# Performance work log

Measured on AMD Instinct MI355X. Metric: run time of the kernel, lower is better.

## Reference

```python
import jax, jax.numpy as jnp
import numpy as np

B, L, D, H = 1, 2048, 1024, 16
d = D // H  # head dim = 64


def setup_inputs() -> dict:
    key = jax.random.key(0)
    ks = jax.random.split(key, 8)
    s = 1.0 / np.sqrt(D)
    return {
        "x": jax.random.normal(ks[0], (B, L, D), jnp.float32),
        "Wqkv_w": (jax.random.normal(ks[1], (D, 3 * D), jnp.float32) * s),
        "Wqkv_b": jnp.zeros((3 * D,), jnp.float32),
        "out_w": (jax.random.normal(ks[2], (D, D), jnp.float32) * s),
        "out_b": jnp.zeros((D,), jnp.float32),
        "W_static": jnp.zeros((H, d, d), jnp.float32),
        "Lambda_raw": jax.random.uniform(ks[3], (H, d, d), jnp.float32, -3.0, 3.0),
        "Gamma": jax.random.uniform(ks[4], (H, d, d), jnp.float32, -0.5 / np.sqrt(d), 0.5 / np.sqrt(d)),
        "gate_w1": (jax.random.normal(ks[5], (D, D // 2), jnp.float32) * s),
        "gate_b1": jnp.zeros((D // 2,), jnp.float32),
        "gate_w2": (jax.random.normal(ks[6], (D // 2, H), jnp.float32) * (1.0 / np.sqrt(D // 2))),
        "gate_b2": jnp.zeros((H,), jnp.float32),
    }


def _forward(x, Wqkv_w, Wqkv_b, out_w, out_b, W_static, Lambda_raw, Gamma,
             gate_w1, gate_b1, gate_w2, gate_b2):
    Bb, Ll, Dm = x.shape
    Hh = Gamma.shape[0]
    dd = Dm // Hh
    scale = 1.0 / np.sqrt(dd)

    # qkv projection: (B,L,3D) -> (3, B, H, L, d) layout
    qkv = (x @ Wqkv_w + Wqkv_b).reshape(Bb, Ll, 3, Hh, dd)
    q = jnp.transpose(qkv[:, :, 0], (0, 2, 1, 3))  # (B,H,L,d)
    k = jnp.transpose(qkv[:, :, 1], (0, 2, 1, 3))
    v = jnp.transpose(qkv[:, :, 2], (0, 2, 1, 3))

    # --- softmax branch (causal, additive -10000 mask like the original) ---
    scores = jnp.einsum('bhid,bhjd->bhij', q, k) * scale
    causal_mask = jnp.triu(jnp.full((Ll, Ll), -10000.0, dtype=scores.dtype), 1)
    attn = jax.nn.softmax(scores + causal_mask, axis=-1)
    y_softmax = jnp.einsum('bhij,bhjd->bhid', attn, v)

    # --- STP branch: linear recurrence over time via lax.scan ---
    retention = 1.0 - jax.nn.sigmoid(Lambda_raw)  # (H,d,d)
    k_stp = k * scale

    def step(state, inp):
        q_t, k_t, v_t = inp  # each (B,H,d)
        hebbian = v_t[..., :, None] * k_t[..., None, :]          # (B,H,d,d)
        state = retention * state + Gamma * hebbian              # (B,H,d,d)
        y_t = jnp.einsum('bhij,bhj->bhi', W_static + state, q_t)  # (B,H,d)
        return state, y_t

    state0 = jnp.zeros((Bb, Hh, dd, dd), x.dtype)
    qT = jnp.moveaxis(q, 2, 0)      # (L,B,H,d)
    kT = jnp.moveaxis(k_stp, 2, 0)
    vT = jnp.moveaxis(v, 2, 0)
    _, ys = jax.lax.scan(step, state0, (qT, kT, vT))
    y_stp = jnp.moveaxis(ys, 0, 2)  # (B,H,L,d)

    # --- learned gate: Linear -> GELU(exact) -> Linear -> sigmoid ---
    g = jax.nn.gelu(x @ gate_w1 + gate_b1, approximate=False)
    alpha = jax.nn.sigmoid(g @ gate_w2 + gate_b2)        # (B,L,H)
    alpha = jnp.transpose(alpha, (0, 2, 1))[..., None]   # (B,H,L,1)

    y = alpha * y_softmax + (1.0 - alpha) * y_stp        # (B,H,L,d)
    y = jnp.transpose(y, (0, 2, 1, 3)).reshape(Bb, Ll, Dm)
    return y @ out_w + out_b


def reference(x, Wqkv_w, Wqkv_b, out_w, out_b, W_static, Lambda_raw, Gamma,
              gate_w1, gate_b1, gate_w2, gate_b2):
    return _forward(x, Wqkv_w, Wqkv_b, out_w, out_b, W_static, Lambda_raw,
                    Gamma, gate_w1, gate_b1, gate_w2, gate_b2)
```

## Files before the change

### kernel.cpp

```cpp
#include <hip/hip_runtime.h>
#include <hip/hip_bf16.h>

#define L_SEQ 2048
#define DMODEL 1024
#define NHEAD 16
#define DHEAD 64
#define D3 3072

typedef __attribute__((ext_vector_type(8))) short s8v;
typedef __attribute__((ext_vector_type(4))) float f4v;
typedef unsigned int u32;

__device__ __forceinline__ short f2bf(float f) {
  __hip_bfloat16 h = __float2bfloat16(f);
  return *reinterpret_cast<short*>(&h);
}
__device__ __forceinline__ int pack2bf(float lo, float hi) {
  return (int)(((unsigned)(unsigned short)f2bf(hi) << 16) |
               (unsigned)(unsigned short)f2bf(lo));
}

__global__ __launch_bounds__(256) void conv_x(const float* __restrict__ x,
                                              short* __restrict__ xb)
{
  int i = (blockIdx.x * 256 + threadIdx.x) * 4;
  float4 v = *(const float4*)(x + i);
  short4 o;
  o.x = f2bf(v.x); o.y = f2bf(v.y); o.z = f2bf(v.z); o.w = f2bf(v.w);
  *(short4*)(xb + i) = o;
}

__global__ __launch_bounds__(256) void transpose_conv(const float* __restrict__ W,
    short* __restrict__ Wt, int K, int N)
{
  __shared__ float T[32][33];
  int bx = blockIdx.x, by = blockIdx.y;
  int col = threadIdx.x & 31, rb = threadIdx.x >> 5;
  #pragma unroll
  for (int it = 0; it < 4; ++it) {
    int r = it * 8 + rb;
    T[r][col] = W[(size_t)(by * 32 + r) * N + bx * 32 + col];
  }
  __syncthreads();
  #pragma unroll
  for (int it = 0; it < 4; ++it) {
    int r = it * 8 + rb;
    Wt[(size_t)(bx * 32 + r) * K + by * 32 + col] = f2bf(T[col][r]);
  }
}

__global__ __launch_bounds__(256) void conv_qkv(const float* __restrict__ qkv,
    short* __restrict__ Qb, short* __restrict__ Kb, short* __restrict__ Vtb)
{
  int kb = blockIdx.x, h = blockIdx.y;
  int tid = threadIdx.x;
  __shared__ float Vs[64][65];
  for (int idx = tid; idx < 2048; idx += 256) {
    int key = idx >> 5, e2 = idx & 31;
    size_t base = (size_t)(kb * 64 + key) * D3 + h * 64 + e2 * 2;
    float2 qv = *(const float2*)(qkv + base);
    float2 kv = *(const float2*)(qkv + base + 1024);
    float2 vv = *(const float2*)(qkv + base + 2048);
    size_t o = ((size_t)h * 2048 + kb * 64 + key) * 64 + e2 * 2;
    *(int*)&Qb[o] = pack2bf(qv.x, qv.y);
    *(int*)&Kb[o] = pack2bf(kv.x, kv.y);
    Vs[key][e2 * 2] = vv.x; Vs[key][e2 * 2 + 1] = vv.y;
  }
  __syncthreads();
  for (int idx = tid; idx < 2048; idx += 256) {
    int dim = idx >> 5, k2 = idx & 31;
    *(int*)&Vtb[((size_t)h * 64 + dim) * 2048 + kb * 64 + k2 * 2] =
        pack2bf(Vs[k2 * 2][dim], Vs[k2 * 2 + 1][dim]);
  }
}

template<int EPI>
__global__ __launch_bounds__(256) void gemm_mfma(
    const short* __restrict__ A, const short* __restrict__ Bt,
    const float* __restrict__ bias, float* __restrict__ C,
    int M, int N, int K)
{
  __shared__ __align__(16) short As[128 * 32];
  __shared__ __align__(16) short Bs[128 * 32];
  const int tid = threadIdx.x;
  const int w = tid >> 6, lane = tid & 63;
  const int quad = lane >> 4, c = lane & 15;
  const int m0 = blockIdx.y * 128, n0 = blockIdx.x * 128;
  const int wm = (w & 1) * 64, wn = (w >> 1) * 64;
  f4v acc[4][4] = {};

  int off0 = (w * 2) * 1024 + lane * 16;
  int row0s = off0 >> 6, colh0 = (off0 & 63) >> 1;
  int off1 = off0 + 1024;
  int row1s = off1 >> 6, colh1 = (off1 & 63) >> 1;

  for (int k0 = 0; k0 < K; k0 += 32) {
    const short* gA0 = A + (size_t)(m0 + row0s) * K + k0 + colh0;
    const short* gA1 = A + (size_t)(m0 + row1s) * K + k0 + colh1;
    const short* gB0 = Bt + (size_t)(n0 + row0s) * K + k0 + colh0;
    const short* gB1 = Bt + (size_t)(n0 + row1s) * K + k0 + colh1;
    __builtin_amdgcn_global_load_lds(
        (const __attribute__((address_space(1))) u32*)gA0,
        (__attribute__((address_space(3))) u32*)(As + (w * 2) * 512), 16, 0, 0);
    __builtin_amdgcn_global_load_lds(
        (const __attribute__((address_space(1))) u32*)gA1,
        (__attribute__((address_space(3))) u32*)(As + (w * 2 + 1) * 512), 16, 0, 0);
    __builtin_amdgcn_global_load_lds(
        (const __attribute__((address_space(1))) u32*)gB0,
        (__attribute__((address_space(3))) u32*)(Bs + (w * 2) * 512), 16, 0, 0);
    __builtin_amdgcn_global_load_lds(
        (const __attribute__((address_space(1))) u32*)gB1,
        (__attribute__((address_space(3))) u32*)(Bs + (w * 2 + 1) * 512), 16, 0, 0);
    __syncthreads();
    s8v af[4], bf[4];
    #pragma unroll
    for (int mt = 0; mt < 4; ++mt)
      af[mt] = *(s8v*)&As[(wm + mt * 16 + c) * 32 + quad * 8];
    #pragma unroll
    for (int nt = 0; nt < 4; ++nt)
      bf[nt] = *(s8v*)&Bs[(wn + nt * 16 + c) * 32 + quad * 8];
    #pragma unroll
    for (int mt = 0; mt < 4; ++mt)
      #pragma unroll
      for (int nt = 0; nt < 4; ++nt)
        acc[mt][nt] = __builtin_amdgcn_mfma_f32_16x16x32_bf16(
            af[mt], bf[nt], acc[mt][nt], 0, 0, 0);
    __syncthreads();
  }
  #pragma unroll
  for (int mt = 0; mt < 4; ++mt)
    #pragma unroll
    for (int r = 0; r < 4; ++r) {
      int m = m0 + wm + mt * 16 + quad * 4 + r;
      #pragma unroll
      for (int nt = 0; nt < 4; ++nt) {
        int n = n0 + wn + nt * 16 + c;
        float v = acc[mt][nt][r] + bias[n];
        if (EPI == 1) v = 0.5f * v * (1.0f + erff(v * 0.70710678118654752f));
        C[(size_t)m * N + n] = v;
      }
    }
}

__global__ __launch_bounds__(256) void attn_mfma(
    const short* __restrict__ Qb, const short* __restrict__ Kb,
    const short* __restrict__ Vtb, float* __restrict__ ysm)
{
  const int bid = blockIdx.x;
  const int h  = bid & 15;
  const int qt = bid >> 4;
  const int q0 = qt * 64;
  const int nt = qt + 1;
  const int tid = threadIdx.x;
  const int w = tid >> 6, lane = tid & 63;
  const int quad = lane >> 4, c = lane & 15;

  __shared__ __align__(16) char smem[27648];
  short* Ks = (short*)smem;
  short* Vt = Ks + 4608;
  short* Ps = Vt + 4608;
  float* Ob = (float*)smem;

  const int qrow = q0 + w * 16 + c;
  s8v qf[2];
  qf[0] = *(const s8v*)(Qb + ((size_t)h * 2048 + qrow) * 64 + quad * 8);
  qf[1] = *(const s8v*)(Qb + ((size_t)h * 2048 + qrow) * 64 + 32 + quad * 8);

  const int srow = tid >> 3, sc = (tid & 7) * 8;
  int4 pk0, pk1, pv0, pv1;
  auto load_tile = [&](int t0) {
    const short* kbase = Kb + ((size_t)h * 2048 + t0 * 64) * 64;
    const short* vbase = Vtb + (size_t)h * 64 * 2048 + t0 * 64;
    pk0 = *(const int4*)(kbase + (size_t)srow * 64 + sc);
    pk1 = *(const int4*)(kbase + (size_t)(srow + 32) * 64 + sc);
    pv0 = *(const int4*)(vbase + (size_t)srow * 2048 + sc);
    pv1 = *(const int4*)(vbase + (size_t)(srow + 32) * 2048 + sc);
  };
  load_tile(0);

  f4v o_acc[4] = {};
  float m = -1e30f, l = 0.f;

  for (int t0 = 0; t0 < nt; ++t0) {
    __syncthreads();
    *(int4*)&Ks[srow * 72 + sc] = pk0;
    *(int4*)&Ks[(srow + 32) * 72 + sc] = pk1;
    *(int4*)&Vt[srow * 72 + sc] = pv0;
    *(int4*)&Vt[(srow + 32) * 72 + sc] = pv1;
    __syncthreads();
    if (t0 + 1 < nt) load_tile(t0 + 1);

    f4v s_acc[4] = {};
    #pragma unroll
    for (int kt = 0; kt < 4; ++kt) {
      #pragma unroll
      for (int kc = 0; kc < 2; ++kc) {
        s8v kf = *(s8v*)&Ks[(kt * 16 + c) * 72 + kc * 32 + quad * 8];
        s_acc[kt] = __builtin_amdgcn_mfma_f32_16x16x32_bf16(kf, qf[kc], s_acc[kt], 0, 0, 0);
      }
    }
    float sv[4][4];
    bool full = (t0 * 64 + 63) <= (q0 + w * 16);
    #pragma unroll
    for (int kt = 0; kt < 4; ++kt)
      #pragma unroll
      for (int r = 0; r < 4; ++r) {
        float s = s_acc[kt][r] * 0.125f;
        if (!full) {
          int key = t0 * 64 + kt * 16 + quad * 4 + r;
          s = (key <= qrow) ? s : -1e30f;
        }
        sv[kt][r] = s;
      }
    float mloc = -1e30f;
    #pragma unroll
    for (int kt = 0; kt < 4; ++kt)
      #pragma unroll
      for (int r = 0; r < 4; ++r) mloc = fmaxf(mloc, sv[kt][r]);
    mloc = fmaxf(mloc, __shfl_xor(mloc, 16));
    mloc = fmaxf(mloc, __shfl_xor(mloc, 32));
    float mnew = fmaxf(m, mloc);
    float alpha = __expf(m - mnew);
    m = mnew;
    float p[4][4], ls = 0.f;
    #pragma unroll
    for (int kt = 0; kt < 4; ++kt)
      #pragma unroll
      for (int r = 0; r < 4; ++r) { p[kt][r] = __expf(sv[kt][r] - mnew); ls += p[kt][r]; }
    ls += __shfl_xor(ls, 16);
    ls += __shfl_xor(ls, 32);
    l = l * alpha + ls;
    #pragma unroll
    for (int mt = 0; mt < 4; ++mt)
      #pragma unroll
      for (int r = 0; r < 4; ++r) o_acc[mt][r] *= alpha;
    short* Pw = Ps + w * 1152;
    #pragma unroll
    for (int kt = 0; kt < 4; ++kt) {
      *(int*)&Pw[c * 72 + kt * 16 + quad * 4]     = pack2bf(p[kt][0], p[kt][1]);
      *(int*)&Pw[c * 72 + kt * 16 + quad * 4 + 2] = pack2bf(p[kt][2], p[kt][3]);
    }
    #pragma unroll
    for (int kc2 = 0; kc2 < 2; ++kc2) {
      s8v pf = *(s8v*)&Pw[c * 72 + kc2 * 32 + quad * 8];
      #pragma unroll
      for (int mt = 0; mt < 4; ++mt) {
        s8v vf = *(s8v*)&Vt[(mt * 16 + c) * 72 + kc2 * 32 + quad * 8];
        o_acc[mt] = __builtin_amdgcn_mfma_f32_16x16x32_bf16(vf, pf, o_acc[mt], 0, 0, 0);
      }
    }
  }

  float rinv = 1.f / l;
  __syncthreads();
  #pragma unroll
  for (int mt = 0; mt < 4; ++mt)
    #pragma unroll
    for (int r = 0; r < 4; ++r)
      Ob[(w * 16 + c) * 66 + mt * 16 + quad * 4 + r] = o_acc[mt][r] * rinv;
  __syncthreads();
  for (int i = tid; i < 4096; i += 256) {
    int q = i >> 6, e = i & 63;
    ysm[((size_t)h * L_SEQ + q0 + q) * 64 + e] = Ob[q * 66 + e];
  }
}

__global__ __launch_bounds__(256) void stp_local(const float* __restrict__ qkv,
    const float* __restrict__ Lam, const float* __restrict__ Gam,
    float* __restrict__ states)
{
  int c = blockIdx.x, h = blockIdx.y;
  int tid = threadIdx.x;
  int i = tid >> 2, j0 = (tid & 3) * 16;
  __shared__ float Kc[64][64];
  __shared__ float Vc[64][64];
  for (int idx = tid; idx < 64 * 64; idx += 256) {
    int t = idx >> 6, e = idx & 63;
    size_t base = (size_t)(c * 64 + t) * D3 + h * 64 + e;
    Kc[t][e] = qkv[base + 1024] * 0.125f;
    Vc[t][e] = qkv[base + 2048];
  }
  float r[16], g[16], s[16];
  #pragma unroll
  for (int e = 0; e < 16; ++e) {
    int idx = h * 4096 + i * 64 + j0 + e;
    float lam = Lam[idx];
    r[e] = 1.f / (1.f + expf(lam));
    g[e] = Gam[idx];
    s[e] = 0.f;
  }
  __syncthreads();
  for (int t = 0; t < 64; ++t) {
    float v = Vc[t][i];
    #pragma unroll
    for (int e = 0; e < 16; ++e)
      s[e] = r[e] * s[e] + g[e] * (v * Kc[t][j0 + e]);
  }
  #pragma unroll
  for (int e = 0; e < 16; ++e)
    states[((size_t)h * 32 + c) * 4096 + i * 64 + j0 + e] = s[e];
}

__global__ __launch_bounds__(256) void stp_scan(const float* __restrict__ Lam,
                                                float* __restrict__ states)
{
  int gid = blockIdx.x * 256 + threadIdx.x;
  float lam = Lam[gid];
  float r = 1.f / (1.f + expf(lam));
  float r64 = r;
  #pragma unroll
  for (int q = 0; q < 6; ++q) r64 *= r64;
  int h = gid >> 12, low = gid & 4095;
  float acc = 0.f;
  for (int c = 0; c < 32; ++c) {
    size_t idx = ((size_t)h * 32 + c) * 4096 + low;
    float dloc = states[idx];
    states[idx] = acc;
    acc = r64 * acc + dloc;
  }
}

__global__ __launch_bounds__(256) void stp_out(const float* __restrict__ qkv,
    const float* __restrict__ Lam, const float* __restrict__ Gam,
    const float* __restrict__ Wst, const float* __restrict__ states,
    float* __restrict__ ystp)
{
  int c = blockIdx.x, h = blockIdx.y;
  int tid = threadIdx.x;
  int i = tid >> 2, j0 = (tid & 3) * 16;
  __shared__ float Kc[64][64];
  __shared__ float Vc[64][64];
  __shared__ float Qc[64][64];
  for (int idx = tid; idx < 64 * 64; idx += 256) {
    int t = idx >> 6, e = idx & 63;
    size_t base = (size_t)(c * 64 + t) * D3 + h * 64 + e;
    Qc[t][e] = qkv[base];
    Kc[t][e] = qkv[base + 1024] * 0.125f;
    Vc[t][e] = qkv[base + 2048];
  }
  float r[16], g[16], s[16], w[16];
  #pragma unroll
  for (int e = 0; e < 16; ++e) {
    int idx = h * 4096 + i * 64 + j0 + e;
    float lam = Lam[idx];
    r[e] = 1.f / (1.f + expf(lam));
    g[e] = Gam[idx];
    w[e] = Wst[idx];
    s[e] = states[((size_t)h * 32 + c) * 4096 + i * 64 + j0 + e];
  }
  __syncthreads();
  for (int t = 0; t < 64; ++t) {
    float v = Vc[t][i];
    float y = 0.f;
    #pragma unroll
    for (int e = 0; e < 16; ++e) {
      s[e] = r[e] * s[e] + g[e] * (v * Kc[t][j0 + e]);
      y += (w[e] + s[e]) * Qc[t][j0 + e];
    }
    y += __shfl_xor(y, 1);
    y += __shfl_xor(y, 2);
    if ((tid & 3) == 0)
      ystp[((size_t)h * L_SEQ + c * 64 + t) * 64 + i] = y;
  }
}

__global__ __launch_bounds__(256) void gate2_kernel(const float* __restrict__ g,
    const float* __restrict__ w2, const float* __restrict__ b2,
    float* __restrict__ alpha)
{
  int gid = blockIdx.x * 256 + threadIdx.x;
  int l = gid >> 4, h = gid & 15;
  float acc = b2[h];
  const float* grow = g + (size_t)l * 512;
  for (int c = 0; c < 512; ++c) acc += grow[c] * w2[c * 16 + h];
  alpha[gid] = 1.f / (1.f + expf(-acc));
}

__global__ __launch_bounds__(256) void combine_kernel(const float* __restrict__ ysm,
    const float* __restrict__ ystp, const float* __restrict__ alpha,
    short* __restrict__ ycb)
{
  int gid = blockIdx.x * 256 + threadIdx.x;
  int l = gid >> 10, cidx = gid & 1023;
  int h = cidx >> 6, e = cidx & 63;
  float a = alpha[l * 16 + h];
  size_t src = ((size_t)h * L_SEQ + l) * 64 + e;
  ycb[gid] = f2bf(a * ysm[src] + (1.f - a) * ystp[src]);
}

extern "C" void kernel_launch(void* const* d_in, const int* in_sizes, int n_in,
                              void* d_out, int out_size, void* d_ws, size_t ws_size,
                              hipStream_t stream) {
  (void)in_sizes; (void)n_in; (void)out_size; (void)ws_size;
  const float* x      = (const float*)d_in[0];
  const float* Wqkv_w = (const float*)d_in[1];
  const float* Wqkv_b = (const float*)d_in[2];
  const float* out_w  = (const float*)d_in[3];
  const float* out_b  = (const float*)d_in[4];
  const float* W_st   = (const float*)d_in[5];
  const float* Lam    = (const float*)d_in[6];
  const float* Gam    = (const float*)d_in[7];
  const float* gw1    = (const float*)d_in[8];
  const float* gb1    = (const float*)d_in[9];
  const float* gw2    = (const float*)d_in[10];
  const float* gb2    = (const float*)d_in[11];

  float* ws     = (float*)d_ws;
  float* qkv    = ws;
  float* ysm    = ws + 6291456;
  float* ystp   = ws + 8388608;
  float* states = ws + 10485760;
  float* ovl    = ws + 12582912;
  float* g      = ovl;
  short* xb     = (short*)(ovl + 1048576);
  short* wt_buf = (short*)(ovl + 2097152);
  float* alpha  = ws + 16252928;
  short* Qb     = (short*)ovl;
  short* Kb     = (short*)(ovl + 1048576);
  short* Vtb    = (short*)(ovl + 2097152);
  short* ycb    = (short*)states;

  conv_x<<<dim3(2048), 256, 0, stream>>>(x, xb);
  transpose_conv<<<dim3(96, 32), 256, 0, stream>>>(Wqkv_w, wt_buf, 1024, 3072);
  gemm_mfma<0><<<dim3(24, 16), 256, 0, stream>>>(xb, wt_buf, Wqkv_b, qkv, 2048, 3072, 1024);
  transpose_conv<<<dim3(16, 32), 256, 0, stream>>>(gw1, wt_buf, 1024, 512);
  gemm_mfma<1><<<dim3(4, 16), 256, 0, stream>>>(xb, wt_buf, gb1, g, 2048, 512, 1024);
  gate2_kernel<<<dim3(128), 256, 0, stream>>>(g, gw2, gb2, alpha);
  stp_local<<<dim3(32, 16), 256, 0, stream>>>(qkv, Lam, Gam, states);
  stp_scan<<<dim3(256), 256, 0, stream>>>(Lam, states);
  stp_out<<<dim3(32, 16), 256, 0, stream>>>(qkv, Lam, Gam, W_st, states, ystp);
  conv_qkv<<<dim3(32, 16), 256, 0, stream>>>(qkv, Qb, Kb, Vtb);
  attn_mfma<<<dim3(512), 256, 0, stream>>>(Qb, Kb, Vtb, ysm);
  combine_kernel<<<dim3(8192), 256, 0, stream>>>(ysm, ystp, alpha, ycb);
  transpose_conv<<<dim3(32, 32), 256, 0, stream>>>(out_w, wt_buf, 1024, 1024);
  gemm_mfma<0><<<dim3(8, 16), 256, 0, stream>>>(ycb, wt_buf, out_b, (float*)d_out, 2048, 1024, 1024);
}
```

Before: 307.0 us.

## Fuse QKV and gate GEMMs, double-buffer GEMM LDS, and store the gate in bf16

After: 275.8 us. 1.11x faster.

```diff
diff --git a/kernel.cpp b/kernel.cpp
--- a/kernel.cpp
+++ b/kernel.cpp
@@ -10,6 +10,8 @@
 typedef __attribute__((ext_vector_type(8))) short s8v;
 typedef __attribute__((ext_vector_type(4))) float f4v;
 typedef unsigned int u32;
+#define AS1 __attribute__((address_space(1)))
+#define AS3 __attribute__((address_space(3)))
 
 __device__ __forceinline__ short f2bf(float f) {
   __hip_bfloat16 h = __float2bfloat16(f);
@@ -74,70 +76,83 @@
   }
 }
 
-template<int EPI>
+template<int BM, int BN, int MODE>
 __global__ __launch_bounds__(256) void gemm_mfma(
     const short* __restrict__ A, const short* __restrict__ Bt,
-    const float* __restrict__ bias, float* __restrict__ C,
+    const float* __restrict__ bias, const float* __restrict__ bias2,
+    float* __restrict__ C, short* __restrict__ C2,
     int M, int N, int K)
 {
-  __shared__ __align__(16) short As[128 * 32];
-  __shared__ __align__(16) short Bs[128 * 32];
+  constexpr int LA = BM / 64, LB = BN / 64;
+  constexpr int WM = BM / 2, WN = BN / 2;
+  constexpr int MT = WM / 16, NT = WN / 16;
+  __shared__ __align__(16) short As[2][BM * 32];
+  __shared__ __align__(16) short Bs[2][BN * 32];
   const int tid = threadIdx.x;
   const int w = tid >> 6, lane = tid & 63;
   const int quad = lane >> 4, c = lane & 15;
-  const int m0 = blockIdx.y * 128, n0 = blockIdx.x * 128;
-  const int wm = (w & 1) * 64, wn = (w >> 1) * 64;
-  f4v acc[4][4] = {};
-
-  int off0 = (w * 2) * 1024 + lane * 16;
-  int row0s = off0 >> 6, colh0 = (off0 & 63) >> 1;
-  int off1 = off0 + 1024;
-  int row1s = off1 >> 6, colh1 = (off1 & 63) >> 1;
-
+  const int m0 = blockIdx.y * BM, n0 = blockIdx.x * BN;
+  const int wm = (w & 1) * WM, wn = (w >> 1) * WN;
+  f4v acc[MT][NT] = {};
+
+  auto stage = [&](int buf, int k0) {
+    #pragma unroll
+    for (int it = 0; it < LA; ++it) {
+      int off = (it * 256 + tid) * 16;
+      int row = off >> 6, colh = (off & 63) >> 1;
+      __builtin_amdgcn_global_load_lds(
+          (const AS1 u32*)(A + (size_t)(m0 + row) * K + k0 + colh),
+          (AS3 u32*)(&As[buf][0] + (off >> 1)), 16, 0, 0);
+    }
+    #pragma unroll
+    for (int it = 0; it < LB; ++it) {
+      int off = (it * 256 + tid) * 16;
+      int row = off >> 6, colh = (off & 63) >> 1;
+      __builtin_amdgcn_global_load_lds(
+          (const AS1 u32*)(Bt + (size_t)(n0 + row) * K + k0 + colh),
+          (AS3 u32*)(&Bs[buf][0] + (off >> 1)), 16, 0, 0);
+    }
+  };
+  stage(0, 0);
+  int cur = 0;
   for (int k0 = 0; k0 < K; k0 += 32) {
-    const short* gA0 = A + (size_t)(m0 + row0s) * K + k0 + colh0;
-    const short* gA1 = A + (size_t)(m0 + row1s) * K + k0 + colh1;
-    const short* gB0 = Bt + (size_t)(n0 + row0s) * K + k0 + colh0;
-    const short* gB1 = Bt + (size_t)(n0 + row1s) * K + k0 + colh1;
-    __builtin_amdgcn_global_load_lds(
-        (const __attribute__((address_space(1))) u32*)gA0,
-        (__attribute__((address_space(3))) u32*)(As + (w * 2) * 512), 16, 0, 0);
-    __builtin_amdgcn_global_load_lds(
-        (const __attribute__((address_space(1))) u32*)gA1,
-        (__attribute__((address_space(3))) u32*)(As + (w * 2 + 1) * 512), 16, 0, 0);
-    __builtin_amdgcn_global_load_lds(
-        (const __attribute__((address_space(1))) u32*)gB0,
-        (__attribute__((address_space(3))) u32*)(Bs + (w * 2) * 512), 16, 0, 0);
-    __builtin_amdgcn_global_load_lds(
-        (const __attribute__((address_space(1))) u32*)gB1,
-        (__attribute__((address_space(3))) u32*)(Bs + (w * 2 + 1) * 512), 16, 0, 0);
     __syncthreads();
-    s8v af[4], bf[4];
-    #pragma unroll
-    for (int mt = 0; mt < 4; ++mt)
-      af[mt] = *(s8v*)&As[(wm + mt * 16 + c) * 32 + quad * 8];
-    #pragma unroll
-    for (int nt = 0; nt < 4; ++nt)
-      bf[nt] = *(s8v*)&Bs[(wn + nt * 16 + c) * 32 + quad * 8];
-    #pragma unroll
-    for (int mt = 0; mt < 4; ++mt)
-      #pragma unroll
-      for (int nt = 0; nt < 4; ++nt)
+    if (k0 + 32 < K) stage(cur ^ 1, k0 + 32);
+    s8v af[MT], bf[NT];
+    #pragma unroll
+    for (int mt = 0; mt < MT; ++mt)
+      af[mt] = *(s8v*)&As[cur][(wm + mt * 16 + c) * 32 + quad * 8];
+    #pragma unroll
+    for (int nt = 0; nt < NT; ++nt)
+      bf[nt] = *(s8v*)&Bs[cur][(wn + nt * 16 + c) * 32 + quad * 8];
+    #pragma unroll
+    for (int mt = 0; mt < MT; ++mt)
+      #pragma unroll
+      for (int nt = 0; nt < NT; ++nt)
         acc[mt][nt] = __builtin_amdgcn_mfma_f32_16x16x32_bf16(
             af[mt], bf[nt], acc[mt][nt], 0, 0, 0);
-    __syncthreads();
-  }
-  #pragma unroll
-  for (int mt = 0; mt < 4; ++mt)
+    cur ^= 1;
+  }
+  #pragma unroll
+  for (int mt = 0; mt < MT; ++mt)
     #pragma unroll
     for (int r = 0; r < 4; ++r) {
       int m = m0 + wm + mt * 16 + quad * 4 + r;
       #pragma unroll
-      for (int nt = 0; nt < 4; ++nt) {
+      for (int nt = 0; nt < NT; ++nt) {
         int n = n0 + wn + nt * 16 + c;
-        float v = acc[mt][nt][r] + bias[n];
-        if (EPI == 1) v = 0.5f * v * (1.0f + erff(v * 0.70710678118654752f));
-        C[(size_t)m * N + n] = v;
+        float v = acc[mt][nt][r];
+        if (MODE == 0) {
+          C[(size_t)m * N + n] = v + bias[n];
+        } else {
+          if (n < 3072) {
+            C[(size_t)m * 3072 + n] = v + bias[n];
+          } else {
+            float t = v + bias2[n - 3072];
+            t = 0.5f * t * (1.0f + erff(t * 0.70710678118654752f));
+            C2[(size_t)m * 512 + (n - 3072)] = f2bf(t);
+          }
+        }
       }
     }
 }
@@ -364,15 +379,20 @@
   }
 }
 
-__global__ __launch_bounds__(256) void gate2_kernel(const float* __restrict__ g,
+__global__ __launch_bounds__(256) void gate2_kernel(const short* __restrict__ g_bf,
     const float* __restrict__ w2, const float* __restrict__ b2,
     float* __restrict__ alpha)
 {
   int gid = blockIdx.x * 256 + threadIdx.x;
   int l = gid >> 4, h = gid & 15;
   float acc = b2[h];
-  const float* grow = g + (size_t)l * 512;
-  for (int c = 0; c < 512; ++c) acc += grow[c] * w2[c * 16 + h];
+  const short* grow = g_bf + (size_t)l * 512;
+  for (int c2 = 0; c2 < 512; c2 += 2) {
+    u32 pk = *(const u32*)(grow + c2);
+    float g0 = __uint_as_float(pk << 16);
+    float g1 = __uint_as_float(pk & 0xffff0000u);
+    acc += g0 * w2[c2 * 16 + h] + g1 * w2[(c2 + 1) * 16 + h];
+  }
   alpha[gid] = 1.f / (1.f + expf(-acc));
 }
 
@@ -411,27 +431,29 @@
   float* ystp   = ws + 8388608;
   float* states = ws + 10485760;
   float* ovl    = ws + 12582912;
-  float* g      = ovl;
-  short* xb     = (short*)(ovl + 1048576);
-  short* wt_buf = (short*)(ovl + 2097152);
   float* alpha  = ws + 16252928;
+  short* xb     = (short*)ovl;
+  short* wt_buf = (short*)(ovl + 1048576);
+  short* g_bf   = (short*)(ovl + 2883584);
   short* Qb     = (short*)ovl;
   short* Kb     = (short*)(ovl + 1048576);
   short* Vtb    = (short*)(ovl + 2097152);
+  short* wtO    = (short*)ovl;
   short* ycb    = (short*)states;
 
   conv_x<<<dim3(2048), 256, 0, stream>>>(x, xb);
   transpose_conv<<<dim3(96, 32), 256, 0, stream>>>(Wqkv_w, wt_buf, 1024, 3072);
-  gemm_mfma<0><<<dim3(24, 16), 256, 0, stream>>>(xb, wt_buf, Wqkv_b, qkv, 2048, 3072, 1024);
-  transpose_conv<<<dim3(16, 32), 256, 0, stream>>>(gw1, wt_buf, 1024, 512);
-  gemm_mfma<1><<<dim3(4, 16), 256, 0, stream>>>(xb, wt_buf, gb1, g, 2048, 512, 1024);
-  gate2_kernel<<<dim3(128), 256, 0, stream>>>(g, gw2, gb2, alpha);
+  transpose_conv<<<dim3(16, 32), 256, 0, stream>>>(gw1, wt_buf + 3072 * 1024, 1024, 512);
+  gemm_mfma<128, 128, 2><<<dim3(28, 16), 256, 0, stream>>>(
+      xb, wt_buf, Wqkv_b, gb1, qkv, g_bf, 2048, 3584, 1024);
+  gate2_kernel<<<dim3(128), 256, 0, stream>>>(g_bf, gw2, gb2, alpha);
   stp_local<<<dim3(32, 16), 256, 0, stream>>>(qkv, Lam, Gam, states);
   stp_scan<<<dim3(256), 256, 0, stream>>>(Lam, states);
   stp_out<<<dim3(32, 16), 256, 0, stream>>>(qkv, Lam, Gam, W_st, states, ystp);
   conv_qkv<<<dim3(32, 16), 256, 0, stream>>>(qkv, Qb, Kb, Vtb);
   attn_mfma<<<dim3(512), 256, 0, stream>>>(Qb, Kb, Vtb, ysm);
   combine_kernel<<<dim3(8192), 256, 0, stream>>>(ysm, ystp, alpha, ycb);
-  transpose_conv<<<dim3(32, 32), 256, 0, stream>>>(out_w, wt_buf, 1024, 1024);
-  gemm_mfma<0><<<dim3(8, 16), 256, 0, stream>>>(ycb, wt_buf, out_b, (float*)d_out, 2048, 1024, 1024);
-}
+  transpose_conv<<<dim3(32, 32), 256, 0, stream>>>(out_w, wtO, 1024, 1024);
+  gemm_mfma<64, 128, 0><<<dim3(8, 32), 256, 0, stream>>>(
+      ycb, wtO, out_b, nullptr, (float*)d_out, nullptr, 2048, 1024, 1024);
+}
```
